# Kernel optimization log

Measured on AMD Instinct MI355X. Metric: run time of the kernel, lower is better.

Reference implementation:

```python
import jax, jax.numpy as jnp
import numpy as np

NUM_CLASSES = 4096
FEAT_DIM = 2048
BATCH = 8192


def setup_inputs() -> dict:
    key = jax.random.key(0)
    kx, kl, kc = jax.random.split(key, 3)
    x = jax.random.normal(kx, (BATCH, FEAT_DIM), dtype=jnp.float32)
    labels = jax.random.randint(kl, (BATCH,), 0, NUM_CLASSES, dtype=jnp.int64)
    centers = jax.random.normal(kc, (NUM_CLASSES, FEAT_DIM), dtype=jnp.float32)
    return {"x": x, "labels": labels, "centers": centers}


def reference(x, labels, centers):
    # distmat[b, c] = ||x_b||^2 + ||center_c||^2 - 2 x_b . center_c
    xf = x.astype(jnp.float32)
    cf = centers.astype(jnp.float32)
    x_sq = jnp.sum(xf * xf, axis=1, keepdims=True)          # (B, 1)
    c_sq = jnp.sum(cf * cf, axis=1)[None, :]                 # (1, C)
    distmat = x_sq + c_sq - 2.0 * (xf @ cf.T)                # (B, C)
    # keep only the entry matching each sample's label class
    mask = (labels[:, None] == jnp.arange(NUM_CLASSES)[None, :]).astype(jnp.float32)
    dist = distmat * mask
    # NOTE: torch clamps the masked matrix, so zeroed entries become 1e-12 and
    # still contribute to the sum — replicated faithfully here.
    loss = jnp.clip(dist, 1e-12, 1e12).sum() / x.shape[0]
    return loss
```

## Files before the change

kernel.cpp:

```cpp
#include <hip/hip_runtime.h>


#define BATCH 8192
#define FEAT  2048
#define NCLS  4096
#define BLK   256
#define WAVES_PER_BLK (BLK / 64)
#define NBLK (BATCH / WAVES_PER_BLK)

__global__ void __launch_bounds__(BLK)
cl_dist(const float* __restrict__ x,
        const int* __restrict__ labels,
        const float* __restrict__ centers,
        float* __restrict__ part) {
    const int tid  = threadIdx.x;
    const int wid  = tid >> 6;
    const int lane = tid & 63;
    const int b    = blockIdx.x * WAVES_PER_BLK + wid;

    const int lbl = labels[b];

    const float4* __restrict__ xr =
        reinterpret_cast<const float4*>(x + (size_t)b * FEAT);
    const float4* __restrict__ cr =
        reinterpret_cast<const float4*>(centers + (size_t)lbl * FEAT);

    float4 xv[8], cv[8];
#pragma unroll
    for (int j = 0; j < 8; ++j) xv[j] = xr[lane + j * 64];
#pragma unroll
    for (int j = 0; j < 8; ++j) cv[j] = cr[lane + j * 64];

    float acc0 = 0.0f, acc1 = 0.0f;
#pragma unroll
    for (int j = 0; j < 8; ++j) {
        const float d0 = xv[j].x - cv[j].x;
        const float d1 = xv[j].y - cv[j].y;
        const float d2 = xv[j].z - cv[j].z;
        const float d3 = xv[j].w - cv[j].w;
        acc0 += d0 * d0 + d1 * d1;
        acc1 += d2 * d2 + d3 * d3;
    }
    float acc = acc0 + acc1;

#pragma unroll
    for (int off = 32; off > 0; off >>= 1)
        acc += __shfl_down(acc, off, 64);

    if (lane == 0) {
        part[b] = fminf(fmaxf(acc, 1e-12f), 1e12f);
    }
}

__global__ void __launch_bounds__(BLK)
cl_final(const float* __restrict__ part, float* __restrict__ out) {
    const int tid = threadIdx.x;
    const float4* __restrict__ pr = reinterpret_cast<const float4*>(part);

    float acc = 0.0f;
#pragma unroll
    for (int j = 0; j < BATCH / 4 / BLK; ++j) {
        const float4 v = pr[tid + j * BLK];
        acc += (v.x + v.y) + (v.z + v.w);
    }

#pragma unroll
    for (int off = 32; off > 0; off >>= 1)
        acc += __shfl_down(acc, off, 64);

    __shared__ float s[BLK / 64];
    const int wid  = tid >> 6;
    const int lane = tid & 63;
    if (lane == 0) s[wid] = acc;
    __syncthreads();

    if (tid == 0) {
        const float total = s[0] + s[1] + s[2] + s[3];
        out[0] = total / (float)BATCH + (float)(NCLS - 1) * 1e-12f;
    }
}

extern "C" void kernel_launch(void* const* d_in, const int* in_sizes, int n_in,
                              void* d_out, int out_size, void* d_ws, size_t ws_size,
                              hipStream_t stream) {
    const float* x       = (const float*)d_in[0];
    const int*   labels  = (const int*)d_in[1];
    const float* centers = (const float*)d_in[2];
    float* out  = (float*)d_out;
    float* part = (float*)d_ws;

    cl_dist<<<NBLK, BLK, 0, stream>>>(x, labels, centers, part);
    cl_final<<<1, BLK, 0, stream>>>(part, out);
}
```

Baseline: 26.33 us.

## Process four samples per wave with double-buffered register prefetch

Cuts the grid from 2048 blocks to 512, so each wave handles four samples instead of one. Loads for the next sample are issued into a second register buffer while the current one is reduced, giving software pipelining across samples. The aim is to lower launch/block overhead and keep more memory requests in flight per wave. The cost is higher register use and fewer waves, which lowers occupancy and could reduce memory-level parallelism.

```diff
diff --git a/kernel.cpp b/kernel.cpp
--- a/kernel.cpp
+++ b/kernel.cpp
@@ -6,7 +6,9 @@
 #define NCLS  4096
 #define BLK   256
 #define WAVES_PER_BLK (BLK / 64)
-#define NBLK (BATCH / WAVES_PER_BLK)
+#define NBLK 512
+#define NWAVE (NBLK * WAVES_PER_BLK)
+#define SPW (BATCH / NWAVE)
 
 __global__ void __launch_bounds__(BLK)
 cl_dist(const float* __restrict__ x,
@@ -16,40 +18,55 @@
     const int tid  = threadIdx.x;
     const int wid  = tid >> 6;
     const int lane = tid & 63;
-    const int b    = blockIdx.x * WAVES_PER_BLK + wid;
+    const int gw   = blockIdx.x * WAVES_PER_BLK + wid;
+    const int b0   = gw * SPW;
 
-    const int lbl = labels[b];
+    float4 xa[8], ca[8], xb[8], cb[8];
 
-    const float4* __restrict__ xr =
-        reinterpret_cast<const float4*>(x + (size_t)b * FEAT);
-    const float4* __restrict__ cr =
-        reinterpret_cast<const float4*>(centers + (size_t)lbl * FEAT);
+#define ISSUE(XBUF, CBUF, S)                                                   \
+    {                                                                          \
+        const float4* __restrict__ xr =                                        \
+            reinterpret_cast<const float4*>(x + (size_t)(b0 + (S)) * FEAT);    \
+        const int lbl = labels[b0 + (S)];                                      \
+        const float4* __restrict__ cr =                                        \
+            reinterpret_cast<const float4*>(centers + (size_t)lbl * FEAT);     \
+        _Pragma("unroll")                                                      \
+        for (int j = 0; j < 8; ++j) XBUF[j] = xr[lane + j * 64];               \
+        _Pragma("unroll")                                                      \
+        for (int j = 0; j < 8; ++j) CBUF[j] = cr[lane + j * 64];               \
+    }
 
-    float4 xv[8], cv[8];
-#pragma unroll
-    for (int j = 0; j < 8; ++j) xv[j] = xr[lane + j * 64];
-#pragma unroll
-    for (int j = 0; j < 8; ++j) cv[j] = cr[lane + j * 64];
+#define COMPUTE(XBUF, CBUF, S)                                                 \
+    {                                                                          \
+        float a0 = 0.0f, a1 = 0.0f;                                            \
+        _Pragma("unroll")                                                      \
+        for (int j = 0; j < 8; ++j) {                                          \
+            const float d0 = XBUF[j].x - CBUF[j].x;                            \
+            const float d1 = XBUF[j].y - CBUF[j].y;                            \
+            const float d2 = XBUF[j].z - CBUF[j].z;                            \
+            const float d3 = XBUF[j].w - CBUF[j].w;                            \
+            a0 += d0 * d0 + d1 * d1;                                           \
+            a1 += d2 * d2 + d3 * d3;                                           \
+        }                                                                      \
+        float acc = a0 + a1;                                                   \
+        _Pragma("unroll")                                                      \
+        for (int off = 32; off > 0; off >>= 1)                                 \
+            acc += __shfl_down(acc, off, 64);                                  \
+        if (lane == 0)                                                         \
+            part[b0 + (S)] = fminf(fmaxf(acc, 1e-12f), 1e12f);                 \
+    }
 
-    float acc0 = 0.0f, acc1 = 0.0f;
-#pragma unroll
-    for (int j = 0; j < 8; ++j) {
-        const float d0 = xv[j].x - cv[j].x;
-        const float d1 = xv[j].y - cv[j].y;
-        const float d2 = xv[j].z - cv[j].z;
-        const float d3 = xv[j].w - cv[j].w;
-        acc0 += d0 * d0 + d1 * d1;
-        acc1 += d2 * d2 + d3 * d3;
-    }
-    float acc = acc0 + acc1;
+    ISSUE(xa, ca, 0);
+    ISSUE(xb, cb, 1);
+    COMPUTE(xa, ca, 0);
+    ISSUE(xa, ca, 2);
+    COMPUTE(xb, cb, 1);
+    ISSUE(xb, cb, 3);
+    COMPUTE(xa, ca, 2);
+    COMPUTE(xb, cb, 3);
 
-#pragma unroll
-    for (int off = 32; off > 0; off >>= 1)
-        acc += __shfl_down(acc, off, 64);
-
-    if (lane == 0) {
-        part[b] = fminf(fmaxf(acc, 1e-12f), 1e12f);
-    }
+#undef ISSUE
+#undef COMPUTE
 }
 
 __global__ void __launch_bounds__(BLK)
```

New measurement: 25.67 us, median of 2. -2.5%, faster.

## Group samples by label to reuse center rows and fuse final reduction

Applied to the files above, without the earlier changes.

Buckets samples by class label with global atomics, then after a grid-wide barrier each wave loads a center row once and computes distances for all samples assigned to that class. The aim is to stop re-reading the same center row from memory for every sample. The separate reduction kernel is folded in through a last-block ticket, and a memset replaces the second launch. The grid barrier depends on all 512 blocks being resident at once. Classes with more than CAP samples fall back to a slow scalar loop.

```diff
diff --git a/kernel.cpp b/kernel.cpp
--- a/kernel.cpp
+++ b/kernel.cpp
@@ -5,78 +5,130 @@
 #define FEAT  2048
 #define NCLS  4096
 #define BLK   256
+#define NBLK  512
+#define CAP   16
 #define WAVES_PER_BLK (BLK / 64)
-#define NBLK (BATCH / WAVES_PER_BLK)
+#define NWAVE (NBLK * WAVES_PER_BLK)
+#define CLS_PER_WAVE (NCLS / NWAVE)
+
+#define OFF_CNT   4
+#define OFF_SLOT  (OFF_CNT + NCLS)
+#define OFF_PART  (OFF_SLOT + NCLS * CAP)
+#define MEMSET_BYTES ((OFF_CNT + NCLS) * 4)
 
 __global__ void __launch_bounds__(BLK)
-cl_dist(const float* __restrict__ x,
-        const int* __restrict__ labels,
-        const float* __restrict__ centers,
-        float* __restrict__ part) {
+cl_all(const float* __restrict__ x,
+       const int* __restrict__ labels,
+       const float* __restrict__ centers,
+       float* __restrict__ out,
+       int* __restrict__ wsi) {
     const int tid  = threadIdx.x;
+    const int bid  = blockIdx.x;
     const int wid  = tid >> 6;
     const int lane = tid & 63;
-    const int b    = blockIdx.x * WAVES_PER_BLK + wid;
 
-    const int lbl = labels[b];
+    int*   __restrict__ cnt   = wsi + OFF_CNT;
+    int*   __restrict__ slots = wsi + OFF_SLOT;
+    float* __restrict__ part  = (float*)(wsi + OFF_PART);
 
-    const float4* __restrict__ xr =
-        reinterpret_cast<const float4*>(x + (size_t)b * FEAT);
-    const float4* __restrict__ cr =
-        reinterpret_cast<const float4*>(centers + (size_t)lbl * FEAT);
+    __shared__ int   sticket;
+    __shared__ float sred[WAVES_PER_BLK];
 
-    float4 xv[8], cv[8];
-#pragma unroll
-    for (int j = 0; j < 8; ++j) xv[j] = xr[lane + j * 64];
-#pragma unroll
-    for (int j = 0; j < 8; ++j) cv[j] = cr[lane + j * 64];
-
-    float acc0 = 0.0f, acc1 = 0.0f;
-#pragma unroll
-    for (int j = 0; j < 8; ++j) {
-        const float d0 = xv[j].x - cv[j].x;
-        const float d1 = xv[j].y - cv[j].y;
-        const float d2 = xv[j].z - cv[j].z;
-        const float d3 = xv[j].w - cv[j].w;
-        acc0 += d0 * d0 + d1 * d1;
-        acc1 += d2 * d2 + d3 * d3;
-    }
-    float acc = acc0 + acc1;
-
-#pragma unroll
-    for (int off = 32; off > 0; off >>= 1)
-        acc += __shfl_down(acc, off, 64);
-
-    if (lane == 0) {
-        part[b] = fminf(fmaxf(acc, 1e-12f), 1e12f);
-    }
-}
-
-__global__ void __launch_bounds__(BLK)
-cl_final(const float* __restrict__ part, float* __restrict__ out) {
-    const int tid = threadIdx.x;
-    const float4* __restrict__ pr = reinterpret_cast<const float4*>(part);
-
-    float acc = 0.0f;
-#pragma unroll
-    for (int j = 0; j < BATCH / 4 / BLK; ++j) {
-        const float4 v = pr[tid + j * BLK];
-        acc += (v.x + v.y) + (v.z + v.w);
+    const int gid = bid * BLK + tid;
+    if (gid < BATCH) {
+        const int l   = labels[gid];
+        const int pos = atomicAdd(&cnt[l], 1);
+        if (pos < CAP) {
+            slots[l * CAP + pos] = gid;
+        } else {
+            const float* xr = x + (size_t)gid * FEAT;
+            const float* cr = centers + (size_t)l * FEAT;
+            float acc = 0.0f;
+            for (int j = 0; j < FEAT; ++j) {
+                const float d = xr[j] - cr[j];
+                acc += d * d;
+            }
+            part[gid] = fminf(fmaxf(acc, 1e-12f), 1e12f);
+        }
     }
 
+    __syncthreads();
+    if (tid == 0) {
+        __builtin_amdgcn_fence(__ATOMIC_RELEASE, "agent");
+        __hip_atomic_fetch_add(&wsi[0], 1, __ATOMIC_ACQ_REL, __HIP_MEMORY_SCOPE_AGENT);
+        while (__hip_atomic_load(&wsi[0], __ATOMIC_ACQUIRE, __HIP_MEMORY_SCOPE_AGENT) < NBLK)
+            __builtin_amdgcn_s_sleep(8);
+    }
+    __syncthreads();
+    __builtin_amdgcn_fence(__ATOMIC_ACQUIRE, "agent");
+
+    const int w = bid * WAVES_PER_BLK + wid;
 #pragma unroll
-    for (int off = 32; off > 0; off >>= 1)
-        acc += __shfl_down(acc, off, 64);
+    for (int k = 0; k < CLS_PER_WAVE; ++k) {
+        const int c  = w * CLS_PER_WAVE + k;
+        const int n0 = cnt[c];
+        if (n0 == 0) continue;
+        const int n = n0 < CAP ? n0 : CAP;
 
-    __shared__ float s[BLK / 64];
-    const int wid  = tid >> 6;
-    const int lane = tid & 63;
-    if (lane == 0) s[wid] = acc;
+        const float4* __restrict__ cr =
+            reinterpret_cast<const float4*>(centers + (size_t)c * FEAT);
+        float4 cv[8];
+#pragma unroll
+        for (int j = 0; j < 8; ++j) cv[j] = cr[lane + j * 64];
+
+        for (int i = 0; i < n; ++i) {
+            const int b = slots[c * CAP + i];
+            const float4* __restrict__ xr =
+                reinterpret_cast<const float4*>(x + (size_t)b * FEAT);
+            float4 xv[8];
+#pragma unroll
+            for (int j = 0; j < 8; ++j) xv[j] = xr[lane + j * 64];
+
+            float a0 = 0.0f, a1 = 0.0f;
+#pragma unroll
+            for (int j = 0; j < 8; ++j) {
+                const float d0 = xv[j].x - cv[j].x;
+                const float d1 = xv[j].y - cv[j].y;
+                const float d2 = xv[j].z - cv[j].z;
+                const float d3 = xv[j].w - cv[j].w;
+                a0 += d0 * d0 + d1 * d1;
+                a1 += d2 * d2 + d3 * d3;
+            }
+            float acc = a0 + a1;
+#pragma unroll
+            for (int off = 32; off > 0; off >>= 1)
+                acc += __shfl_down(acc, off, 64);
+            if (lane == 0)
+                part[b] = fminf(fmaxf(acc, 1e-12f), 1e12f);
+        }
+    }
+
+    __syncthreads();
+    if (tid == 0) {
+        __builtin_amdgcn_fence(__ATOMIC_RELEASE, "agent");
+        sticket = __hip_atomic_fetch_add(&wsi[1], 1, __ATOMIC_ACQ_REL,
+                                         __HIP_MEMORY_SCOPE_AGENT);
+    }
     __syncthreads();
 
-    if (tid == 0) {
-        const float total = s[0] + s[1] + s[2] + s[3];
-        out[0] = total / (float)BATCH + (float)(NCLS - 1) * 1e-12f;
+    if (sticket == NBLK - 1) {
+        __builtin_amdgcn_fence(__ATOMIC_ACQUIRE, "agent");
+        const float4* __restrict__ pr = reinterpret_cast<const float4*>(part);
+        float acc = 0.0f;
+#pragma unroll
+        for (int j = 0; j < BATCH / 4 / BLK; ++j) {
+            const float4 v = pr[tid + j * BLK];
+            acc += (v.x + v.y) + (v.z + v.w);
+        }
+#pragma unroll
+        for (int off = 32; off > 0; off >>= 1)
+            acc += __shfl_down(acc, off, 64);
+        if (lane == 0) sred[wid] = acc;
+        __syncthreads();
+        if (tid == 0) {
+            const float total = sred[0] + sred[1] + sred[2] + sred[3];
+            out[0] = total / (float)BATCH + (float)(NCLS - 1) * 1e-12f;
+        }
     }
 }
 
@@ -86,9 +138,9 @@
     const float* x       = (const float*)d_in[0];
     const int*   labels  = (const int*)d_in[1];
     const float* centers = (const float*)d_in[2];
-    float* out  = (float*)d_out;
-    float* part = (float*)d_ws;
+    float* out = (float*)d_out;
+    int*   wsi = (int*)d_ws;
 
-    cl_dist<<<NBLK, BLK, 0, stream>>>(x, labels, centers, part);
-    cl_final<<<1, BLK, 0, stream>>>(part, out);
+    (void)hipMemsetAsync(d_ws, 0, MEMSET_BYTES, stream);
+    cl_all<<<NBLK, BLK, 0, stream>>>(x, labels, centers, out, wsi);
 }
```

New measurement: 95.15 us. 3.61x slower.
